# Optimization experiments

Hardware: AMD Instinct MI355X
Metric: run time of the kernel (lower is better)

## Reference

```python
import jax, jax.numpy as jnp
import numpy as np

_T_DURATION = 0.2
_C = 0.206756


def setup_inputs() -> dict:
    key = jax.random.key(0)
    k1, k2, k3, k4 = jax.random.split(key, 4)
    B, Nt = 512, 32768
    # normalised params (unused by the analytic path, kept for signature fidelity)
    h = jax.random.normal(k1, (B, 3), dtype=jnp.float32)
    # uniform time grid over the PFWD pulse duration [0, 0.2] s
    t = jnp.linspace(0.0, _T_DURATION, Nt, dtype=jnp.float32)
    # pressure history ~ typical PFWD peak 150 kPa, non-negative half-sine-ish pulse
    u = jax.random.uniform(k2, (B, Nt), dtype=jnp.float32)
    pulse = jnp.sin(jnp.pi * t / _T_DURATION)[None, :]  # (1, Nt) in [0,1]
    p = 150000.0 * pulse * (0.8 + 0.4 * u)  # Pa, peak ~150 kPa
    # physical params inside documented ranges: E1 [1e8,2e9], E2 [1e7,2e8], eta [1e4,5e6]
    r = jax.random.uniform(k3, (B, 3), dtype=jnp.float32)
    lo = jnp.array([1.0e8, 1.0e7, 1.0e4], dtype=jnp.float32)
    hi = jnp.array([2.0e9, 2.0e8, 5.0e6], dtype=jnp.float32)
    h_raw = lo + r * (hi - lo)
    return {"h": h, "t": t, "p": p, "h_raw": h_raw}


def reference(h, t, p, h_raw):
    """omega_i = sum_{j<=i} g(t_i - t_j) * dp_j,
    g(tau) = C*[1/(E1+E2) + E1/(E2*(E1+E2))*(1 - exp(-alpha*tau))],
    alpha  = E1*E2 / ((E1+E2)*eta).
    Exact O(Nt) reformulation: g = (A+D) - D*exp(-alpha*tau) with
    A = C/(E1+E2), D = C*E1/(E2*(E1+E2)), so
    omega_i = (A+D)*p_i - D*s_i,  s_i = exp(-alpha*dt_i)*s_{i-1} + dp_i.
    """
    E1, E2, eta = h_raw[:, 0], h_raw[:, 1], h_raw[:, 2]  # (B,)
    alpha = E1 * E2 / ((E1 + E2) * eta)                   # (B,)
    A = _C / (E1 + E2)                                    # (B,)
    D = _C * E1 / (E2 * (E1 + E2))                        # (B,)
    dp = jnp.diff(p, axis=1, prepend=0.0)                 # (B, Nt), dp_0 = p_0
    dt = jnp.diff(t, prepend=t[0])                        # (Nt,),  dt_0 = 0
    decay = jnp.exp(-alpha[:, None] * dt[None, :])        # (B, Nt)

    def step(s, xs):
        d, dpi = xs                                       # each (B,)
        s = d * s + dpi
        return s, s

    s0 = jnp.zeros(p.shape[0], dtype=p.dtype)
    _, s = jax.lax.scan(step, s0, (decay.T, dp.T))        # s: (Nt, B)
    s = s.T                                               # (B, Nt)
    omega = (A + D)[:, None] * p - D[:, None] * s         # (B, Nt), metres
    return omega
```

## Files before the change

### kernel.cpp

```cpp
#include <hip/hip_runtime.h>

#define TPB 512
#define ROUNDS 16
#define NCHUNK 4
#define RPC (ROUNDS / NCHUNK)
#define WAVE 64
#define NW (TPB / WAVE)

__global__ __launch_bounds__(TPB, 4)
void fused_scan(const float* __restrict__ tt, const float* __restrict__ p,
                const float* __restrict__ h_raw, float* __restrict__ out, int Nt)
{
    const int row  = blockIdx.x;
    const int t    = threadIdx.x;
    const int lane = t & (WAVE - 1);
    const int wid  = t >> 6;

    const float E1  = h_raw[row * 3 + 0];
    const float E2  = h_raw[row * 3 + 1];
    const float eta = h_raw[row * 3 + 2];
    const float alpha = (E1 * E2) / ((E1 + E2) * eta);
    const float A = 0.206756f / (E1 + E2);
    const float D = 0.206756f * E1 / (E2 * (E1 + E2));
    const float dtm = (tt[Nt - 1] - tt[0]) / (float)(Nt - 1);
    const float omd = -expm1f(-alpha * dtm);
    const float d   = 1.0f - omd;
    const float K1  = (A + D) - D / d;
    const float K2  = D * omd / d;

    const float d4 = (d * d) * (d * d);
    float d256 = d4;
    #pragma unroll
    for (int i = 0; i < 6; ++i) d256 *= d256;
    float d2048 = d256;
    d2048 *= d2048; d2048 *= d2048; d2048 *= d2048;
    float d4l = 1.0f;
    {
        float b = d4;
        #pragma unroll
        for (int i = 0; i < 6; ++i) { if (lane & (1 << i)) d4l *= b; b *= b; }
    }
    float d256w = 1.0f;
    {
        float b = d256;
        #pragma unroll
        for (int i = 0; i < 3; ++i) { if (wid & (1 << i)) d256w *= b; b *= b; }
    }

    const long long base = (long long)row * (long long)Nt;
    const float4* pg = reinterpret_cast<const float4*>(p + base);
    float4*       og = reinterpret_cast<float4*>(out + base);

    float4 v[ROUNDS];
    #pragma unroll
    for (int r = 0; r < ROUNDS; ++r) v[r] = pg[r * TPB + t];

    __shared__ float sw[2][RPC][NW];

    float C = 0.0f;

    #pragma unroll
    for (int c = 0; c < NCHUNK; ++c) {
        float x[RPC], wex[RPC];
        #pragma unroll
        for (int j = 0; j < RPC; ++j) {
            const float4 pv = v[c * RPC + j];
            x[j] = fmaf(fmaf(fmaf(pv.x, d, pv.y), d, pv.z), d, pv.w);
        }

        float m = d4;
        #pragma unroll
        for (int k = 1; k < WAVE; k <<= 1) {
            #pragma unroll
            for (int j = 0; j < RPC; ++j) {
                const float y = __shfl_up(x[j], k);
                if (lane >= k) x[j] = fmaf(m, y, x[j]);
            }
            m *= m;
        }
        #pragma unroll
        for (int j = 0; j < RPC; ++j) {
            wex[j] = __shfl_up(x[j], 1);
            if (lane == 0) wex[j] = 0.0f;
        }

        if (lane == WAVE - 1) {
            #pragma unroll
            for (int j = 0; j < RPC; ++j) sw[c & 1][j][wid] = x[j];
        }
        __syncthreads();

        #pragma unroll
        for (int j = 0; j < RPC; ++j) {
            const float4 sA = *reinterpret_cast<const float4*>(&sw[c & 1][j][0]);
            const float4 sB = *reinterpret_cast<const float4*>(&sw[c & 1][j][4]);
            float run = 0.0f, E = 0.0f;
            #define STEP(w, val) { if (wid == (w)) E = run; run = fmaf(d256, run, (val)); }
            STEP(0, sA.x) STEP(1, sA.y) STEP(2, sA.z) STEP(3, sA.w)
            STEP(4, sB.x) STEP(5, sB.y) STEP(6, sB.z) STEP(7, sB.w)
            #undef STEP
            const float Bt = run;

            const float seed = fmaf(fmaf(C, d256w, E), d4l, wex[j]);

            const float4 pv = v[c * RPC + j];
            float W = seed;
            float4 o;
            W = fmaf(W, d, pv.x); o.x = fmaf(K2, W, K1 * pv.x);
            W = fmaf(W, d, pv.y); o.y = fmaf(K2, W, K1 * pv.y);
            W = fmaf(W, d, pv.z); o.z = fmaf(K2, W, K1 * pv.z);
            W = fmaf(W, d, pv.w); o.w = fmaf(K2, W, K1 * pv.w);
            og[(c * RPC + j) * TPB + t] = o;

            C = fmaf(d2048, C, Bt);
        }
    }
}

extern "C" void kernel_launch(void* const* d_in, const int* in_sizes, int n_in,
                              void* d_out, int out_size, void* d_ws, size_t ws_size,
                              hipStream_t stream)
{
    const float* tt    = (const float*)d_in[1];
    const float* p     = (const float*)d_in[2];
    const float* h_raw = (const float*)d_in[3];
    float* out = (float*)d_out;

    const int Nt = in_sizes[1];
    const int B  = in_sizes[2] / Nt;
    if (Nt != ROUNDS * TPB * 4) return;

    fused_scan<<<B, TPB, 0, stream>>>(tt, p, h_raw, out, Nt);
}
```

Baseline: 24.22 us.

## Double-buffer chunk loads, derive exclusive scan algebraically, raise occupancy bound

Instead of loading all 16 float4 rounds into registers up front, the kernel now loads one chunk ahead into a two-slot register buffer, which cuts register pressure. Launch bounds are raised to 6 blocks per SM. The shuffle that produced the exclusive wave prefix is replaced by computing (inclusive - own) * 1/d^4. That removes shuffles but adds a division whose result can lose precision or go unstable when d^4 is tiny.

```diff
diff --git a/kernel.cpp b/kernel.cpp
--- a/kernel.cpp
+++ b/kernel.cpp
@@ -7,7 +7,7 @@
 #define WAVE 64
 #define NW (TPB / WAVE)
 
-__global__ __launch_bounds__(TPB, 4)
+__global__ __launch_bounds__(TPB, 6)
 void fused_scan(const float* __restrict__ tt, const float* __restrict__ p,
                 const float* __restrict__ h_raw, float* __restrict__ out, int Nt)
 {
@@ -29,6 +29,7 @@
     const float K2  = D * omd / d;
 
     const float d4 = (d * d) * (d * d);
+    const float inv_d4 = 1.0f / d4;
     float d256 = d4;
     #pragma unroll
     for (int i = 0; i < 6; ++i) d256 *= d256;
@@ -51,21 +52,30 @@
     const float4* pg = reinterpret_cast<const float4*>(p + base);
     float4*       og = reinterpret_cast<float4*>(out + base);
 
-    float4 v[ROUNDS];
+    __shared__ float sw[2][RPC][NW];
+
+    float4 v[2][RPC];
     #pragma unroll
-    for (int r = 0; r < ROUNDS; ++r) v[r] = pg[r * TPB + t];
-
-    __shared__ float sw[2][RPC][NW];
+    for (int j = 0; j < RPC; ++j) v[0][j] = pg[j * TPB + t];
 
     float C = 0.0f;
 
     #pragma unroll
     for (int c = 0; c < NCHUNK; ++c) {
-        float x[RPC], wex[RPC];
+        const int cb = c & 1, nb = cb ^ 1;
+
+        if (c + 1 < NCHUNK) {
+            #pragma unroll
+            for (int j = 0; j < RPC; ++j)
+                v[nb][j] = pg[((c + 1) * RPC + j) * TPB + t];
+        }
+
+        float x[RPC], T[RPC];
         #pragma unroll
         for (int j = 0; j < RPC; ++j) {
-            const float4 pv = v[c * RPC + j];
-            x[j] = fmaf(fmaf(fmaf(pv.x, d, pv.y), d, pv.z), d, pv.w);
+            const float4 pv = v[cb][j];
+            T[j] = fmaf(fmaf(fmaf(pv.x, d, pv.y), d, pv.z), d, pv.w);
+            x[j] = T[j];
         }
 
         float m = d4;
@@ -78,22 +88,17 @@
             }
             m *= m;
         }
-        #pragma unroll
-        for (int j = 0; j < RPC; ++j) {
-            wex[j] = __shfl_up(x[j], 1);
-            if (lane == 0) wex[j] = 0.0f;
-        }
 
         if (lane == WAVE - 1) {
             #pragma unroll
-            for (int j = 0; j < RPC; ++j) sw[c & 1][j][wid] = x[j];
+            for (int j = 0; j < RPC; ++j) sw[cb][j][wid] = x[j];
         }
         __syncthreads();
 
         #pragma unroll
         for (int j = 0; j < RPC; ++j) {
-            const float4 sA = *reinterpret_cast<const float4*>(&sw[c & 1][j][0]);
-            const float4 sB = *reinterpret_cast<const float4*>(&sw[c & 1][j][4]);
+            const float4 sA = *reinterpret_cast<const float4*>(&sw[cb][j][0]);
+            const float4 sB = *reinterpret_cast<const float4*>(&sw[cb][j][4]);
             float run = 0.0f, E = 0.0f;
             #define STEP(w, val) { if (wid == (w)) E = run; run = fmaf(d256, run, (val)); }
             STEP(0, sA.x) STEP(1, sA.y) STEP(2, sA.z) STEP(3, sA.w)
@@ -101,9 +106,11 @@
             #undef STEP
             const float Bt = run;
 
-            const float seed = fmaf(fmaf(C, d256w, E), d4l, wex[j]);
+            const float wexcl = (x[j] - T[j]) * inv_d4;
 
-            const float4 pv = v[c * RPC + j];
+            const float seed = fmaf(fmaf(C, d256w, E), d4l, wexcl);
+
+            const float4 pv = v[cb][j];
             float W = seed;
             float4 o;
             W = fmaf(W, d, pv.x); o.x = fmaf(K2, W, K1 * pv.x);
```

After: 26.10 us. +7.8%, slower.
